# Kernel optimization log

Hardware: AMD Instinct MI355X
Metric: run time of the kernel (lower is better)

## Reference

```python
import jax, jax.numpy as jnp
import numpy as np


def setup_inputs() -> dict:
    key = jax.random.key(0)
    ks = jax.random.split(key, 8)
    B, N, M, H = 8192, 2048, 2048, 10
    return {
        "X": jax.random.normal(ks[0], (B, N), dtype=jnp.float32),
        "weight": jax.random.normal(ks[1], (N, M), dtype=jnp.float32),
        "W1": jax.random.normal(ks[2], (3, H), dtype=jnp.float32) * 0.5,
        "b1": jax.random.normal(ks[3], (H,), dtype=jnp.float32) * 0.1,
        "W2": jax.random.normal(ks[4], (H, H), dtype=jnp.float32) * 0.3,
        "b2": jax.random.normal(ks[5], (H,), dtype=jnp.float32) * 0.1,
        "W3": jax.random.normal(ks[6], (H, 1), dtype=jnp.float32) * 0.3,
        "b3": jax.random.normal(ks[7], (1,), dtype=jnp.float32) * 0.1,
    }


def reference(X, weight, W1, b1, W2, b2, W3, b3):
    # NCA local rule, vectorized over all (i, j) cells.
    # 'forward'  = mean of column j excluding row i  (leave-one-out col mean)
    # 'backward' = mean of row i excluding column j  (leave-one-out row mean)
    n, m = weight.shape
    col_sum = jnp.sum(weight, axis=0, keepdims=True)            # [1, m]
    row_sum = jnp.sum(weight, axis=1, keepdims=True)            # [n, 1]
    fwd_mean = (col_sum - weight) / jnp.float32(n - 1)          # [n, m]
    bwd_mean = (row_sum - weight) / jnp.float32(m - 1)          # [n, m]
    feats = jnp.stack([weight, fwd_mean, bwd_mean], axis=-1)    # [n, m, 3]
    # tiny 3 -> 10 -> 10 -> 1 MLP applied per cell
    h = jax.nn.relu(feats @ W1 + b1)                            # [n, m, 10]
    h = jax.nn.relu(h @ W2 + b2)                                # [n, m, 10]
    updates = (h @ W3 + b3)[..., 0]                             # [n, m]
    new_weight = weight + updates
    # forward: softmax(X @ W)
    return jax.nn.softmax(X @ new_weight, axis=-1)
```

## Files before the change

### kernel.cpp

```cpp
#include <hip/hip_runtime.h>
#include <hip/hip_bf16.h>


typedef int int4v __attribute__((ext_vector_type(4)));
typedef int int16v __attribute__((ext_vector_type(16)));

#define GK 2048
#define NROWS 2048
#define MCOLS 2048
#define NCHUNK 16

#define CS_BLOCKS 128
#define RS_BLOCKS 2048
__global__ __launch_bounds__(256) void pre_kernel(
    const float* __restrict__ X, const float* __restrict__ W,
    signed char* __restrict__ X1, signed char* __restrict__ X2,
    float* __restrict__ sx1,
    float* __restrict__ part, float* __restrict__ rowS) {
  const int bid = blockIdx.x;
  const int tid = threadIdx.x;

  if (bid < CS_BLOCKS) {
    int chunk = bid >> 3;
    int j = (bid & 7) * 256 + tid;
    int i0 = chunk * (NROWS / NCHUNK);
    float s = 0.f;
    for (int i = i0; i < i0 + NROWS / NCHUNK; ++i) s += W[(size_t)i * MCOLS + j];
    part[(size_t)chunk * MCOLS + j] = s;
    return;
  }
  if (bid < CS_BLOCKS + RS_BLOCKS) {
    int row = bid - CS_BLOCKS;
    const float4* p = (const float4*)(W + (size_t)row * MCOLS);
    float4 a = p[tid];
    float4 b = p[tid + 256];
    float v = (a.x + a.y) + (a.z + a.w) + (b.x + b.y) + (b.z + b.w);
    __shared__ float red[256];
    red[tid] = v;
    __syncthreads();
    for (int s = 128; s > 0; s >>= 1) {
      if (tid < s) red[tid] += red[tid + s];
      __syncthreads();
    }
    if (tid == 0) rowS[row] = red[0];
    return;
  }
  {
    int row = bid - CS_BLOCKS - RS_BLOCKS;
    const float4* xr = (const float4*)(X + (size_t)row * GK);
    float4 a = xr[tid * 2];
    float4 b = xr[tid * 2 + 1];
    float xs[8] = {a.x, a.y, a.z, a.w, b.x, b.y, b.z, b.w};
    float am = 0.f;
#pragma unroll
    for (int i = 0; i < 8; ++i) am = fmaxf(am, fabsf(xs[i]));
    const int lane = tid & 63, wv = tid >> 6;
#pragma unroll
    for (int off = 32; off > 0; off >>= 1)
      am = fmaxf(am, __shfl_xor(am, off));
    __shared__ float wred[4];
    if (lane == 0) wred[wv] = am;
    __syncthreads();
    float amax = fmaxf(fmaxf(wred[0], wred[1]), fmaxf(wred[2], wred[3]));
    float s1 = amax * (1.0f / 127.0f);
    float inv = 127.0f / amax;
    int q1[8], q2[8];
#pragma unroll
    for (int i = 0; i < 8; ++i) {
      q1[i] = (int)rintf(xs[i] * inv);
      float r = xs[i] - (float)q1[i] * s1;
      q2[i] = (int)rintf(r * (254.0f * inv));
    }
    unsigned lo1 = (q1[0] & 255) | ((q1[1] & 255) << 8) | ((q1[2] & 255) << 16) | ((q1[3] & 255) << 24);
    unsigned hi1 = (q1[4] & 255) | ((q1[5] & 255) << 8) | ((q1[6] & 255) << 16) | ((q1[7] & 255) << 24);
    unsigned lo2 = (q2[0] & 255) | ((q2[1] & 255) << 8) | ((q2[2] & 255) << 16) | ((q2[3] & 255) << 24);
    unsigned hi2 = (q2[4] & 255) | ((q2[5] & 255) << 8) | ((q2[6] & 255) << 16) | ((q2[7] & 255) << 24);
    ((uint2*)(X1 + (size_t)row * GK))[tid] = make_uint2(lo1, hi1);
    ((uint2*)(X2 + (size_t)row * GK))[tid] = make_uint2(lo2, hi2);
    if (tid == 0) sx1[row] = s1;
  }
}

__global__ __launch_bounds__(256) void nca_update_kernel(
    const float* __restrict__ W, const float* __restrict__ part,
    const float* __restrict__ rowS,
    const float* __restrict__ W1, const float* __restrict__ b1,
    const float* __restrict__ W2, const float* __restrict__ b2,
    const float* __restrict__ W3, const float* __restrict__ b3,
    float* __restrict__ Wt) {
  __shared__ float sW1[30], sb1[10], sW2[100], sb2[10], sW3[10], sb3;
  __shared__ float sColS[32];
  __shared__ float cred[NCHUNK][33];
  __shared__ float Tf[32][33];
  const int tid = threadIdx.x;
  const int i0 = blockIdx.y * 32;
  const int j0 = blockIdx.x * 32;

  if (tid < 30) sW1[tid] = W1[tid];
  if (tid < 10) { sb1[tid] = b1[tid]; sb2[tid] = b2[tid]; sW3[tid] = W3[tid]; }
  if (tid >= 32 && tid < 132) sW2[tid - 32] = W2[tid - 32];
  if (tid == 0) sb3 = b3[0];

  {
    int ch = tid >> 5;
    int jl = tid & 31;
    cred[ch][jl]     = part[(size_t)ch * MCOLS + j0 + jl];
    cred[ch + 8][jl] = part[(size_t)(ch + 8) * MCOLS + j0 + jl];
  }
  __syncthreads();
  if (tid < 32) {
    float s = 0.f;
#pragma unroll
    for (int c = 0; c < NCHUNK; ++c) s += cred[c][tid];
    sColS[tid] = s;
  }
  __syncthreads();

  const int r = tid >> 5;
  const int c = tid & 31;

  float w[4], fwd[4], bwd[4];
#pragma unroll
  for (int cell = 0; cell < 4; ++cell) {
    int il = r + 8 * cell;
    float wv = W[(size_t)(i0 + il) * MCOLS + j0 + c];
    w[cell] = wv;
    fwd[cell] = (sColS[c] - wv) * (1.0f / (float)(NROWS - 1));
    bwd[cell] = (rowS[i0 + il] - wv) * (1.0f / (float)(MCOLS - 1));
  }

  float h1[4][10];
#pragma unroll
  for (int o = 0; o < 10; ++o) {
    float w1a = sW1[o], w1b = sW1[10 + o], w1c = sW1[20 + o], bb = sb1[o];
#pragma unroll
    for (int cell = 0; cell < 4; ++cell) {
      float v = fmaf(w[cell], w1a, fmaf(fwd[cell], w1b, fmaf(bwd[cell], w1c, bb)));
      h1[cell][o] = fmaxf(v, 0.f);
    }
  }
  float u[4] = {sb3, sb3, sb3, sb3};
#pragma unroll
  for (int o = 0; o < 10; ++o) {
    float h2[4];
    float bb = sb2[o];
#pragma unroll
    for (int cell = 0; cell < 4; ++cell) h2[cell] = bb;
#pragma unroll
    for (int p = 0; p < 10; ++p) {
      float wv = sW2[p * 10 + o];
#pragma unroll
      for (int cell = 0; cell < 4; ++cell) h2[cell] = fmaf(h1[cell][p], wv, h2[cell]);
    }
    float w3 = sW3[o];
#pragma unroll
    for (int cell = 0; cell < 4; ++cell) u[cell] = fmaf(fmaxf(h2[cell], 0.f), w3, u[cell]);
  }

#pragma unroll
  for (int cell = 0; cell < 4; ++cell) {
    int il = r + 8 * cell;
    Tf[il][c] = w[cell] + u[cell];
  }
  __syncthreads();

  {
    int r2 = tid >> 4;
    int ic = (tid & 15) * 2;
#pragma unroll
    for (int half = 0; half < 2; ++half) {
      int jl = r2 + 16 * half;
      float2 v = make_float2(Tf[ic][jl], Tf[ic + 1][jl]);
      *(float2*)(&Wt[(size_t)(j0 + jl) * NROWS + i0 + ic]) = v;
    }
  }
}

__global__ __launch_bounds__(256) void bquant_kernel(
    const float* __restrict__ Wt, signed char* __restrict__ B1,
    signed char* __restrict__ B2, float* __restrict__ sw1) {
  const int row = blockIdx.x;
  const int tid = threadIdx.x;
  const float4* wr = (const float4*)(Wt + (size_t)row * GK);
  float4 a = wr[tid * 2];
  float4 b = wr[tid * 2 + 1];
  float xs[8] = {a.x, a.y, a.z, a.w, b.x, b.y, b.z, b.w};
  float am = 0.f;
#pragma unroll
  for (int i = 0; i < 8; ++i) am = fmaxf(am, fabsf(xs[i]));
  const int lane = tid & 63, wv = tid >> 6;
#pragma unroll
  for (int off = 32; off > 0; off >>= 1)
    am = fmaxf(am, __shfl_xor(am, off));
  __shared__ float wred[4];
  if (lane == 0) wred[wv] = am;
  __syncthreads();
  float amax = fmaxf(fmaxf(wred[0], wred[1]), fmaxf(wred[2], wred[3]));
  float s1 = amax * (1.0f / 127.0f);
  float inv = 127.0f / amax;
  int q1[8], q2[8];
#pragma unroll
  for (int i = 0; i < 8; ++i) {
    q1[i] = (int)rintf(xs[i] * inv);
    float r = xs[i] - (float)q1[i] * s1;
    q2[i] = (int)rintf(r * (254.0f * inv));
  }
  unsigned lo1 = (q1[0] & 255) | ((q1[1] & 255) << 8) | ((q1[2] & 255) << 16) | ((q1[3] & 255) << 24);
  unsigned hi1 = (q1[4] & 255) | ((q1[5] & 255) << 8) | ((q1[6] & 255) << 16) | ((q1[7] & 255) << 24);
  unsigned lo2 = (q2[0] & 255) | ((q2[1] & 255) << 8) | ((q2[2] & 255) << 16) | ((q2[3] & 255) << 24);
  unsigned hi2 = (q2[4] & 255) | ((q2[5] & 255) << 8) | ((q2[6] & 255) << 16) | ((q2[7] & 255) << 24);
  ((uint2*)(B1 + (size_t)row * GK))[tid] = make_uint2(lo1, hi1);
  ((uint2*)(B2 + (size_t)row * GK))[tid] = make_uint2(lo2, hi2);
  if (tid == 0) sw1[row] = s1;
}

__global__ __launch_bounds__(256, 2) void gemm_kernel(
    const signed char* __restrict__ X1, const signed char* __restrict__ X2,
    const signed char* __restrict__ B1, const signed char* __restrict__ B2,
    const float* __restrict__ sw1, float* __restrict__ C) {
  __shared__ __align__(16) char sL[32768];

  const int tid = threadIdx.x;
  const int lane = tid & 63;
  const int wave = tid >> 6;
  const int wr = wave >> 1;
  const int wc = wave & 1;

  const int bx = blockIdx.x;
  const int by = blockIdx.y;

  const signed char* A1g = X1 + (size_t)(by * 128) * GK;
  const signed char* A2g = X2 + (size_t)(by * 128) * GK;
  const signed char* B1g = B1 + (size_t)(bx * 128) * GK;
  const signed char* B2g = B2 + (size_t)(bx * 128) * GK;

  const int srow = lane >> 2;
  const int skof = ((lane & 3) ^ ((lane >> 3) & 3)) * 16;

  const int rl = lane & 15;
  const int fhalf = (lane >> 4) & 1;
  const int fck = lane >> 5;

  int aoff[2][2], boff[2][2];
#pragma unroll
  for (int t = 0; t < 2; ++t)
#pragma unroll
    for (int ks = 0; ks < 2; ++ks) {
      int c = 2 * ks + fck;
      int slot = 4 * rl + (c ^ ((rl >> 1) & 3));
      aoff[t][ks] = (wr * 4 + t * 2 + fhalf) * 1024 + slot * 16;
      boff[t][ks] = (wc * 4 + t * 2 + fhalf) * 1024 + slot * 16;
    }

  int16v acc_h[2][2], acc_c[2][2];
#pragma unroll
  for (int i = 0; i < 2; ++i)
#pragma unroll
    for (int j = 0; j < 2; ++j)
#pragma unroll
      for (int e = 0; e < 16; ++e) { acc_h[i][j][e] = 0; acc_c[i][j][e] = 0; }

  for (int k0 = 0; k0 < GK; k0 += 64) {
#pragma unroll
    for (int r = 0; r < 2; ++r) {
      int R = wave * 2 + r;
      size_t goff = (size_t)(R * 16 + srow) * GK + k0 + skof;
      int ldsoff = R * 1024;
      __builtin_amdgcn_global_load_lds(
          (const __attribute__((address_space(1))) void*)(A1g + goff),
          (__attribute__((address_space(3))) void*)(sL + ldsoff), 16, 0, 0);
      __builtin_amdgcn_global_load_lds(
          (const __attribute__((address_space(1))) void*)(A2g + goff),
          (__attribute__((address_space(3))) void*)(sL + 8192 + ldsoff), 16, 0, 0);
      __builtin_amdgcn_global_load_lds(
          (const __attribute__((address_space(1))) void*)(B1g + goff),
          (__attribute__((address_space(3))) void*)(sL + 16384 + ldsoff), 16, 0, 0);
      __builtin_amdgcn_global_load_lds(
          (const __attribute__((address_space(1))) void*)(B2g + goff),
          (__attribute__((address_space(3))) void*)(sL + 24576 + ldsoff), 16, 0, 0);
    }
    __syncthreads();

    int4v a1[2][2], a2[2][2];
#pragma unroll
    for (int mi = 0; mi < 2; ++mi)
#pragma unroll
      for (int ks = 0; ks < 2; ++ks) {
        a1[mi][ks] = *(const int4v*)(sL + aoff[mi][ks]);
        a2[mi][ks] = *(const int4v*)(sL + 8192 + aoff[mi][ks]);
      }
#pragma unroll
    for (int ni = 0; ni < 2; ++ni)
#pragma unroll
      for (int ks = 0; ks < 2; ++ks) {
        int4v b1f = *(const int4v*)(sL + 16384 + boff[ni][ks]);
        int4v b2f = *(const int4v*)(sL + 24576 + boff[ni][ks]);
#pragma unroll
        for (int mi = 0; mi < 2; ++mi) {
          acc_h[mi][ni] = __builtin_amdgcn_mfma_i32_32x32x32_i8(a1[mi][ks], b1f, acc_h[mi][ni], 0, 0, 0);
          acc_c[mi][ni] = __builtin_amdgcn_mfma_i32_32x32x32_i8(a1[mi][ks], b2f, acc_c[mi][ni], 0, 0, 0);
          acc_c[mi][ni] = __builtin_amdgcn_mfma_i32_32x32x32_i8(a2[mi][ks], b1f, acc_c[mi][ni], 0, 0, 0);
        }
      }
    __syncthreads();
  }

  const int ecol = lane & 31;
  const int erow = 4 * (lane >> 5);
#pragma unroll
  for (int ni = 0; ni < 2; ++ni) {
    int col = bx * 128 + wc * 64 + ni * 32 + ecol;
    float sw = sw1[col];
#pragma unroll
    for (int mi = 0; mi < 2; ++mi) {
#pragma unroll
      for (int reg = 0; reg < 16; ++reg) {
        int row = by * 128 + wr * 64 + mi * 32 + (reg & 3) + 8 * (reg >> 2) + erow;
        float v = (float)acc_h[mi][ni][reg] + (float)acc_c[mi][ni][reg] * (1.0f / 254.0f);
        C[(size_t)row * 2048 + col] = v * sw;
      }
    }
  }
}

__global__ __launch_bounds__(256) void softmax_kernel(
    float* __restrict__ C, const float* __restrict__ sx1) {
  const int lane = threadIdx.x & 63;
  const int wv = threadIdx.x >> 6;
  const int row = blockIdx.x * 4 + wv;
  const float sx = sx1[row];
  float4* p = (float4*)(C + (size_t)row * MCOLS);

  float4 v[8];
#pragma unroll
  for (int j = 0; j < 8; ++j) {
    v[j] = p[j * 64 + lane];
    v[j].x *= sx; v[j].y *= sx; v[j].z *= sx; v[j].w *= sx;
  }

  float vmax = -3.4e38f;
#pragma unroll
  for (int j = 0; j < 8; ++j)
    vmax = fmaxf(vmax, fmaxf(fmaxf(v[j].x, v[j].y), fmaxf(v[j].z, v[j].w)));
#pragma unroll
  for (int off = 32; off > 0; off >>= 1)
    vmax = fmaxf(vmax, __shfl_xor(vmax, off));

  float sum = 0.f;
#pragma unroll
  for (int j = 0; j < 8; ++j) {
    v[j].x = __expf(v[j].x - vmax);
    v[j].y = __expf(v[j].y - vmax);
    v[j].z = __expf(v[j].z - vmax);
    v[j].w = __expf(v[j].w - vmax);
    sum += (v[j].x + v[j].y) + (v[j].z + v[j].w);
  }
#pragma unroll
  for (int off = 32; off > 0; off >>= 1)
    sum += __shfl_xor(sum, off);
  float inv = 1.0f / sum;

#pragma unroll
  for (int j = 0; j < 8; ++j) {
    v[j].x *= inv; v[j].y *= inv; v[j].z *= inv; v[j].w *= inv;
    p[j * 64 + lane] = v[j];
  }
}

extern "C" void kernel_launch(void* const* d_in, const int* in_sizes, int n_in,
                              void* d_out, int out_size, void* d_ws, size_t ws_size,
                              hipStream_t stream) {
  const float* X      = (const float*)d_in[0];
  const float* weight = (const float*)d_in[1];
  const float* W1     = (const float*)d_in[2];
  const float* b1     = (const float*)d_in[3];
  const float* W2     = (const float*)d_in[4];
  const float* b2     = (const float*)d_in[5];
  const float* W3     = (const float*)d_in[6];
  const float* b3     = (const float*)d_in[7];
  float* out = (float*)d_out;

  const int N = 2048, M = 2048;
  const int Bdim = in_sizes[0] / N;

  float* rowS = (float*)d_ws;
  float* part = rowS + 2048;
  float* sx1  = part + NCHUNK * 2048;
  float* sw1  = sx1 + 8192;
  float* Wt   = sw1 + 2048;
  signed char* X1 = (signed char*)(Wt + (size_t)M * N);
  signed char* X2 = X1 + (size_t)Bdim * N;
  signed char* B1q = X2 + (size_t)Bdim * N;
  signed char* B2q = B1q + (size_t)M * N;

  pre_kernel<<<CS_BLOCKS + RS_BLOCKS + Bdim, 256, 0, stream>>>(
      X, weight, X1, X2, sx1, part, rowS);

  nca_update_kernel<<<dim3(M / 32, N / 32), 256, 0, stream>>>(
      weight, part, rowS, W1, b1, W2, b2, W3, b3, Wt);

  bquant_kernel<<<M, 256, 0, stream>>>(Wt, B1q, B2q, sw1);

  gemm_kernel<<<dim3(M / 128, Bdim / 128), 256, 0, stream>>>(
      X1, X2, B1q, B2q, sw1, out);

  softmax_kernel<<<Bdim / 4, 256, 0, stream>>>(out, sx1);
}
```

Baseline: 289.3 us.

## Pre-pack B in MFMA fragment layout and double-buffer A tiles in LDS

The bquant kernel now writes the quantized weight in a layout that matches the MFMA fragments, so the GEMM loads B operands straight from global memory into registers. Only the A tiles are staged through LDS, and they are double-buffered so each iteration needs one barrier instead of two. The change also adds scheduling priority and group barriers, widens the column-sum pass to more blocks, and reads the MLP weights directly instead of copying them to shared memory. The risk is that B is now read per wave without LDS sharing, which raises global and L2 traffic.

```diff
diff --git a/kernel.cpp b/kernel.cpp
--- a/kernel.cpp
+++ b/kernel.cpp
@@ -10,7 +10,7 @@
 #define MCOLS 2048
 #define NCHUNK 16
 
-#define CS_BLOCKS 128
+#define CS_BLOCKS 512
 #define RS_BLOCKS 2048
 __global__ __launch_bounds__(256) void pre_kernel(
     const float* __restrict__ X, const float* __restrict__ W,
@@ -21,12 +21,18 @@
   const int tid = threadIdx.x;
 
   if (bid < CS_BLOCKS) {
-    int chunk = bid >> 3;
-    int j = (bid & 7) * 256 + tid;
-    int i0 = chunk * (NROWS / NCHUNK);
+    int chunk = bid >> 5;
+    int j0 = (bid & 31) * 64;
+    int c = tid & 63, q = tid >> 6;
+    int i0 = chunk * 128 + q * 32;
     float s = 0.f;
-    for (int i = i0; i < i0 + NROWS / NCHUNK; ++i) s += W[(size_t)i * MCOLS + j];
-    part[(size_t)chunk * MCOLS + j] = s;
+    for (int i = 0; i < 32; ++i) s += W[(size_t)(i0 + i) * MCOLS + j0 + c];
+    __shared__ float red[4][64];
+    red[q][c] = s;
+    __syncthreads();
+    if (tid < 64)
+      part[(size_t)chunk * MCOLS + j0 + tid] =
+          (red[0][tid] + red[1][tid]) + (red[2][tid] + red[3][tid]);
     return;
   }
   if (bid < CS_BLOCKS + RS_BLOCKS) {
@@ -88,7 +94,6 @@
     const float* __restrict__ W2, const float* __restrict__ b2,
     const float* __restrict__ W3, const float* __restrict__ b3,
     float* __restrict__ Wt) {
-  __shared__ float sW1[30], sb1[10], sW2[100], sb2[10], sW3[10], sb3;
   __shared__ float sColS[32];
   __shared__ float cred[NCHUNK][33];
   __shared__ float Tf[32][33];
@@ -96,11 +101,6 @@
   const int i0 = blockIdx.y * 32;
   const int j0 = blockIdx.x * 32;
 
-  if (tid < 30) sW1[tid] = W1[tid];
-  if (tid < 10) { sb1[tid] = b1[tid]; sb2[tid] = b2[tid]; sW3[tid] = W3[tid]; }
-  if (tid >= 32 && tid < 132) sW2[tid - 32] = W2[tid - 32];
-  if (tid == 0) sb3 = b3[0];
-
   {
     int ch = tid >> 5;
     int jl = tid & 31;
@@ -132,27 +132,28 @@
   float h1[4][10];
 #pragma unroll
   for (int o = 0; o < 10; ++o) {
-    float w1a = sW1[o], w1b = sW1[10 + o], w1c = sW1[20 + o], bb = sb1[o];
+    float w1a = W1[o], w1b = W1[10 + o], w1c = W1[20 + o], bb = b1[o];
 #pragma unroll
     for (int cell = 0; cell < 4; ++cell) {
       float v = fmaf(w[cell], w1a, fmaf(fwd[cell], w1b, fmaf(bwd[cell], w1c, bb)));
       h1[cell][o] = fmaxf(v, 0.f);
     }
   }
-  float u[4] = {sb3, sb3, sb3, sb3};
+  const float b3v = b3[0];
+  float u[4] = {b3v, b3v, b3v, b3v};
 #pragma unroll
   for (int o = 0; o < 10; ++o) {
     float h2[4];
-    float bb = sb2[o];
+    float bb = b2[o];
 #pragma unroll
     for (int cell = 0; cell < 4; ++cell) h2[cell] = bb;
 #pragma unroll
     for (int p = 0; p < 10; ++p) {
-      float wv = sW2[p * 10 + o];
+      float wv = W2[p * 10 + o];
 #pragma unroll
       for (int cell = 0; cell < 4; ++cell) h2[cell] = fmaf(h1[cell][p], wv, h2[cell]);
     }
-    float w3 = sW3[o];
+    float w3 = W3[o];
 #pragma unroll
     for (int cell = 0; cell < 4; ++cell) u[cell] = fmaf(fmaxf(h2[cell], 0.f), w3, u[cell]);
   }
@@ -179,46 +180,97 @@
 __global__ __launch_bounds__(256) void bquant_kernel(
     const float* __restrict__ Wt, signed char* __restrict__ B1,
     signed char* __restrict__ B2, float* __restrict__ sw1) {
-  const int row = blockIdx.x;
   const int tid = threadIdx.x;
-  const float4* wr = (const float4*)(Wt + (size_t)row * GK);
-  float4 a = wr[tid * 2];
-  float4 b = wr[tid * 2 + 1];
-  float xs[8] = {a.x, a.y, a.z, a.w, b.x, b.y, b.z, b.w};
+  const int lane = tid & 63, wv = tid >> 6;
+  const int rb = blockIdx.x;
+  const int row = rb * 4 + wv;
+  const float4* wr = (const float4*)(Wt + (size_t)row * GK) + lane * 8;
+  float xs[32];
+#pragma unroll
+  for (int i = 0; i < 8; ++i) {
+    float4 t = wr[i];
+    xs[i * 4 + 0] = t.x; xs[i * 4 + 1] = t.y;
+    xs[i * 4 + 2] = t.z; xs[i * 4 + 3] = t.w;
+  }
   float am = 0.f;
 #pragma unroll
-  for (int i = 0; i < 8; ++i) am = fmaxf(am, fabsf(xs[i]));
-  const int lane = tid & 63, wv = tid >> 6;
+  for (int i = 0; i < 32; ++i) am = fmaxf(am, fabsf(xs[i]));
 #pragma unroll
   for (int off = 32; off > 0; off >>= 1)
     am = fmaxf(am, __shfl_xor(am, off));
-  __shared__ float wred[4];
-  if (lane == 0) wred[wv] = am;
+  float s1 = am * (1.0f / 127.0f);
+  float inv = 127.0f / am;
+  unsigned w1[8], w2[8];
+#pragma unroll
+  for (int i = 0; i < 8; ++i) { w1[i] = 0u; w2[i] = 0u; }
+#pragma unroll
+  for (int i = 0; i < 32; ++i) {
+    int q1 = (int)rintf(xs[i] * inv);
+    float r = xs[i] - (float)q1 * s1;
+    int q2 = (int)rintf(r * (254.0f * inv));
+    w1[i >> 2] |= (unsigned)(q1 & 255) << ((i & 3) * 8);
+    w2[i >> 2] |= (unsigned)(q2 & 255) << ((i & 3) * 8);
+  }
+  int4v v1lo = {(int)w1[0], (int)w1[1], (int)w1[2], (int)w1[3]};
+  int4v v1hi = {(int)w1[4], (int)w1[5], (int)w1[6], (int)w1[7]};
+  int4v v2lo = {(int)w2[0], (int)w2[1], (int)w2[2], (int)w2[3]};
+  int4v v2hi = {(int)w2[4], (int)w2[5], (int)w2[6], (int)w2[7]};
+  __shared__ int4v tr[4][2][2][65];
+  tr[wv][0][0][lane] = v1lo;
+  tr[wv][0][1][lane] = v1hi;
+  tr[wv][1][0][lane] = v2lo;
+  tr[wv][1][1][lane] = v2hi;
+  if (lane == 0) sw1[row] = s1;
   __syncthreads();
-  float amax = fmaxf(fmaxf(wred[0], wred[1]), fmaxf(wred[2], wred[3]));
-  float s1 = amax * (1.0f / 127.0f);
-  float inv = 127.0f / amax;
-  int q1[8], q2[8];
-#pragma unroll
-  for (int i = 0; i < 8; ++i) {
-    q1[i] = (int)rintf(xs[i] * inv);
-    float r = xs[i] - (float)q1[i] * s1;
-    q2[i] = (int)rintf(r * (254.0f * inv));
-  }
-  unsigned lo1 = (q1[0] & 255) | ((q1[1] & 255) << 8) | ((q1[2] & 255) << 16) | ((q1[3] & 255) << 24);
-  unsigned hi1 = (q1[4] & 255) | ((q1[5] & 255) << 8) | ((q1[6] & 255) << 16) | ((q1[7] & 255) << 24);
-  unsigned lo2 = (q2[0] & 255) | ((q2[1] & 255) << 8) | ((q2[2] & 255) << 16) | ((q2[3] & 255) << 24);
-  unsigned hi2 = (q2[4] & 255) | ((q2[5] & 255) << 8) | ((q2[6] & 255) << 16) | ((q2[7] & 255) << 24);
-  ((uint2*)(B1 + (size_t)row * GK))[tid] = make_uint2(lo1, hi1);
-  ((uint2*)(B2 + (size_t)row * GK))[tid] = make_uint2(lo2, hi2);
-  if (tid == 0) sw1[row] = s1;
-}
+  const int k = tid >> 2, r = tid & 3;
+  const int n32 = rb >> 3;
+  const int nl0 = (rb * 4) & 31;
+  int4v* d1 = (int4v*)B1 + ((size_t)n32 * 64 + k) * 64;
+  int4v* d2 = (int4v*)B2 + ((size_t)n32 * 64 + k) * 64;
+  d1[nl0 + r]      = tr[r][0][0][k];
+  d1[nl0 + r + 32] = tr[r][0][1][k];
+  d2[nl0 + r]      = tr[r][1][0][k];
+  d2[nl0 + r + 32] = tr[r][1][1][k];
+}
+
+#define BM 128
+#define BN 128
+#define BK 64
+#define NT (GK / BK)
+
+__device__ __forceinline__ void glds16(const signed char* g, char* l) {
+  __builtin_amdgcn_global_load_lds(
+      (const __attribute__((address_space(1))) void*)g,
+      (__attribute__((address_space(3))) void*)l, 16, 0, 0);
+}
+
+#define MFMA_I8 __builtin_amdgcn_mfma_i32_32x32x32_i8
+
+#define STAGEA(buf, koff)                                                      \
+  glds16(gA0 + (koff), (buf) + swb0);                                          \
+  glds16(gA1 + (koff), (buf) + swb1);                                          \
+  glds16(gA2 + (koff), (buf) + swb2);                                          \
+  glds16(gA3 + (koff), (buf) + swb3);
+
+#define MM12(ks)                                                               \
+  acc_h[0][0] = MFMA_I8(a1f[0][ks], b1f[0][ks], acc_h[0][0], 0, 0, 0);         \
+  acc_h[0][1] = MFMA_I8(a1f[0][ks], b1f[1][ks], acc_h[0][1], 0, 0, 0);         \
+  acc_h[1][0] = MFMA_I8(a1f[1][ks], b1f[0][ks], acc_h[1][0], 0, 0, 0);         \
+  acc_h[1][1] = MFMA_I8(a1f[1][ks], b1f[1][ks], acc_h[1][1], 0, 0, 0);         \
+  acc_c[0][0] = MFMA_I8(a1f[0][ks], b2f[0][ks], acc_c[0][0], 0, 0, 0);         \
+  acc_c[0][1] = MFMA_I8(a1f[0][ks], b2f[1][ks], acc_c[0][1], 0, 0, 0);         \
+  acc_c[1][0] = MFMA_I8(a1f[1][ks], b2f[0][ks], acc_c[1][0], 0, 0, 0);         \
+  acc_c[1][1] = MFMA_I8(a1f[1][ks], b2f[1][ks], acc_c[1][1], 0, 0, 0);         \
+  acc_c[0][0] = MFMA_I8(a2f[0][ks], b1f[0][ks], acc_c[0][0], 0, 0, 0);         \
+  acc_c[0][1] = MFMA_I8(a2f[0][ks], b1f[1][ks], acc_c[0][1], 0, 0, 0);         \
+  acc_c[1][0] = MFMA_I8(a2f[1][ks], b1f[0][ks], acc_c[1][0], 0, 0, 0);         \
+  acc_c[1][1] = MFMA_I8(a2f[1][ks], b1f[1][ks], acc_c[1][1], 0, 0, 0);
 
 __global__ __launch_bounds__(256, 2) void gemm_kernel(
     const signed char* __restrict__ X1, const signed char* __restrict__ X2,
-    const signed char* __restrict__ B1, const signed char* __restrict__ B2,
+    const int4v* __restrict__ B1p, const int4v* __restrict__ B2p,
     const float* __restrict__ sw1, float* __restrict__ C) {
-  __shared__ __align__(16) char sL[32768];
+  __shared__ __align__(16) char sA[2][16384];
 
   const int tid = threadIdx.x;
   const int lane = tid & 63;
@@ -229,28 +281,37 @@
   const int bx = blockIdx.x;
   const int by = blockIdx.y;
 
-  const signed char* A1g = X1 + (size_t)(by * 128) * GK;
-  const signed char* A2g = X2 + (size_t)(by * 128) * GK;
-  const signed char* B1g = B1 + (size_t)(bx * 128) * GK;
-  const signed char* B2g = B2 + (size_t)(bx * 128) * GK;
+  const signed char* A1g = X1 + (size_t)(by * BM) * GK;
+  const signed char* A2g = X2 + (size_t)(by * BM) * GK;
 
   const int srow = lane >> 2;
-  const int skof = ((lane & 3) ^ ((lane >> 3) & 3)) * 16;
+  const int schk = (lane & 3) ^ ((lane >> 3) & 3);
+  const int b0 = wave * 4;
+  const signed char* gAbase = (b0 >= 8) ? A2g : A1g;
+  const signed char* gA0 = gAbase + (size_t)(((b0 + 0) & 7) * 16 + srow) * GK + schk * 16;
+  const signed char* gA1 = gAbase + (size_t)(((b0 + 1) & 7) * 16 + srow) * GK + schk * 16;
+  const signed char* gA2 = gAbase + (size_t)(((b0 + 2) & 7) * 16 + srow) * GK + schk * 16;
+  const signed char* gA3 = gAbase + (size_t)(((b0 + 3) & 7) * 16 + srow) * GK + schk * 16;
+  const int swb0 = (b0 + 0) * 1024;
+  const int swb1 = (b0 + 1) * 1024;
+  const int swb2 = (b0 + 2) * 1024;
+  const int swb3 = (b0 + 3) * 1024;
 
   const int rl = lane & 15;
   const int fhalf = (lane >> 4) & 1;
   const int fck = lane >> 5;
-
-  int aoff[2][2], boff[2][2];
-#pragma unroll
-  for (int t = 0; t < 2; ++t)
+  int aoff[2][2];
+#pragma unroll
+  for (int mi = 0; mi < 2; ++mi)
 #pragma unroll
     for (int ks = 0; ks < 2; ++ks) {
       int c = 2 * ks + fck;
       int slot = 4 * rl + (c ^ ((rl >> 1) & 3));
-      aoff[t][ks] = (wr * 4 + t * 2 + fhalf) * 1024 + slot * 16;
-      boff[t][ks] = (wc * 4 + t * 2 + fhalf) * 1024 + slot * 16;
-    }
+      aoff[mi][ks] = (wr * 4 + mi * 2 + fhalf) * 1024 + slot * 16;
+    }
+
+  const size_t bb0 = ((size_t)(bx * 4 + wc * 2 + 0) * 64) * 64 + lane;
+  const size_t bb1 = ((size_t)(bx * 4 + wc * 2 + 1) * 64) * 64 + lane;
 
   int16v acc_h[2][2], acc_c[2][2];
 #pragma unroll
@@ -260,64 +321,59 @@
 #pragma unroll
       for (int e = 0; e < 16; ++e) { acc_h[i][j][e] = 0; acc_c[i][j][e] = 0; }
 
-  for (int k0 = 0; k0 < GK; k0 += 64) {
-#pragma unroll
-    for (int r = 0; r < 2; ++r) {
-      int R = wave * 2 + r;
-      size_t goff = (size_t)(R * 16 + srow) * GK + k0 + skof;
-      int ldsoff = R * 1024;
-      __builtin_amdgcn_global_load_lds(
-          (const __attribute__((address_space(1))) void*)(A1g + goff),
-          (__attribute__((address_space(3))) void*)(sL + ldsoff), 16, 0, 0);
-      __builtin_amdgcn_global_load_lds(
-          (const __attribute__((address_space(1))) void*)(A2g + goff),
-          (__attribute__((address_space(3))) void*)(sL + 8192 + ldsoff), 16, 0, 0);
-      __builtin_amdgcn_global_load_lds(
-          (const __attribute__((address_space(1))) void*)(B1g + goff),
-          (__attribute__((address_space(3))) void*)(sL + 16384 + ldsoff), 16, 0, 0);
-      __builtin_amdgcn_global_load_lds(
-          (const __attribute__((address_space(1))) void*)(B2g + goff),
-          (__attribute__((address_space(3))) void*)(sL + 24576 + ldsoff), 16, 0, 0);
-    }
+  STAGEA(sA[0], 0);
+
+#pragma unroll 1
+  for (int kt = 0; kt < NT; ++kt) {
+    const char* rb = sA[kt & 1];
+    char* wb = (char*)sA[(kt + 1) & 1];
     __syncthreads();
-
-    int4v a1[2][2], a2[2][2];
+    if (kt + 1 < NT) { STAGEA(wb, (size_t)(kt + 1) * BK); }
+
+    int4v b1f[2][2], b2f[2][2];
+#pragma unroll
+    for (int ks = 0; ks < 2; ++ks) {
+      size_t ko = (size_t)(kt * 2 + ks) * 64;
+      b1f[0][ks] = B1p[bb0 + ko];
+      b1f[1][ks] = B1p[bb1 + ko];
+      b2f[0][ks] = B2p[bb0 + ko];
+      b2f[1][ks] = B2p[bb1 + ko];
+    }
+    int4v a1f[2][2], a2f[2][2];
 #pragma unroll
     for (int mi = 0; mi < 2; ++mi)
 #pragma unroll
       for (int ks = 0; ks < 2; ++ks) {
-        a1[mi][ks] = *(const int4v*)(sL + aoff[mi][ks]);
-        a2[mi][ks] = *(const int4v*)(sL + 8192 + aoff[mi][ks]);
+        a1f[mi][ks] = *(const int4v*)(rb + aoff[mi][ks]);
+        a2f[mi][ks] = *(const int4v*)(rb + aoff[mi][ks] + 8192);
       }
-#pragma unroll
-    for (int ni = 0; ni < 2; ++ni)
-#pragma unroll
-      for (int ks = 0; ks < 2; ++ks) {
-        int4v b1f = *(const int4v*)(sL + 16384 + boff[ni][ks]);
-        int4v b2f = *(const int4v*)(sL + 24576 + boff[ni][ks]);
-#pragma unroll
-        for (int mi = 0; mi < 2; ++mi) {
-          acc_h[mi][ni] = __builtin_amdgcn_mfma_i32_32x32x32_i8(a1[mi][ks], b1f, acc_h[mi][ni], 0, 0, 0);
-          acc_c[mi][ni] = __builtin_amdgcn_mfma_i32_32x32x32_i8(a1[mi][ks], b2f, acc_c[mi][ni], 0, 0, 0);
-          acc_c[mi][ni] = __builtin_amdgcn_mfma_i32_32x32x32_i8(a2[mi][ks], b1f, acc_c[mi][ni], 0, 0, 0);
-        }
-      }
-    __syncthreads();
+
+    __builtin_amdgcn_s_setprio(1);
+    MM12(0);
+    MM12(1);
+    __builtin_amdgcn_s_setprio(0);
+
+#pragma unroll
+    for (int g = 0; g < 8; ++g) {
+      __builtin_amdgcn_sched_group_barrier(0x100, 1, 0);
+      __builtin_amdgcn_sched_group_barrier(0x020, 1, 0);
+      __builtin_amdgcn_sched_group_barrier(0x008, 3, 0);
+    }
   }
 
   const int ecol = lane & 31;
   const int erow = 4 * (lane >> 5);
 #pragma unroll
   for (int ni = 0; ni < 2; ++ni) {
-    int col = bx * 128 + wc * 64 + ni * 32 + ecol;
+    int col = bx * BN + wc * 64 + ni * 32 + ecol;
     float sw = sw1[col];
 #pragma unroll
     for (int mi = 0; mi < 2; ++mi) {
 #pragma unroll
       for (int reg = 0; reg < 16; ++reg) {
-        int row = by * 128 + wr * 64 + mi * 32 + (reg & 3) + 8 * (reg >> 2) + erow;
+        int row = by * BM + wr * 64 + mi * 32 + (reg & 3) + 8 * (reg >> 2) + erow;
         float v = (float)acc_h[mi][ni][reg] + (float)acc_c[mi][ni][reg] * (1.0f / 254.0f);
-        C[(size_t)row * 2048 + col] = v * sw;
+        C[(size_t)row * MCOLS + col] = v * sw;
       }
     }
   }
@@ -399,10 +455,10 @@
   nca_update_kernel<<<dim3(M / 32, N / 32), 256, 0, stream>>>(
       weight, part, rowS, W1, b1, W2, b2, W3, b3, Wt);
 
-  bquant_kernel<<<M, 256, 0, stream>>>(Wt, B1q, B2q, sw1);
-
-  gemm_kernel<<<dim3(M / 128, Bdim / 128), 256, 0, stream>>>(
-      X1, X2, B1q, B2q, sw1, out);
+  bquant_kernel<<<M / 4, 256, 0, stream>>>(Wt, B1q, B2q, sw1);
+
+  gemm_kernel<<<dim3(M / BN, Bdim / BM), 256, 0, stream>>>(
+      X1, X2, (const int4v*)B1q, (const int4v*)B2q, sw1, out);
 
   softmax_kernel<<<Bdim / 4, 256, 0, stream>>>(out, sx1);
 }
```

New measurement: 306.7 us. +6.0%, slower.
